# Kernel tuning notes

Measured on AMD Instinct MI355X. Metric: run time of the kernel, lower is better.

Reference implementation:

```python
import jax, jax.numpy as jnp
import numpy as np

HIDDEN = 1024
HEADS = 16
HEAD_DIM = 64
FFN = 4096
LAYERS = 8
QLEN = 9
PATCH = 4
PREFIX = PATCH + 1
LATENT = 64
NSTEPS = 4


def _rope_tables():
    # matches __init__: cos/sin for positions 0..QLEN-1, sin first half negated
    half = HEAD_DIM // 2
    inv = 1.0 / (10000.0 ** (np.arange(half, dtype=np.float64) / half))
    ang = np.arange(QLEN)[:, None] * inv[None, :]          # [QLEN, half]
    cos = np.concatenate([np.cos(ang), np.cos(ang)], -1)   # [QLEN, HEAD_DIM]
    sin = np.concatenate([-np.sin(ang), np.sin(ang)], -1)  # first half *= -1
    return jnp.asarray(cos, jnp.float32), jnp.asarray(sin, jnp.float32)

ROPE_COS, ROPE_SIN = _rope_tables()


def _rms(x):
    # norm weight * sqrt(hidden) is folded into the following projection
    return x * jax.lax.rsqrt(jnp.sum(x * x, -1, keepdims=True))


def setup_inputs() -> dict:
    key = jax.random.key(0)
    ks = jax.random.split(key, 16)
    s = 0.02
    return {
        "step": 2,
        "random": jax.random.normal(ks[0], (1, PATCH, LATENT), jnp.float32),
        "dit_hidden": jax.random.normal(ks[1], (1, 1, HIDDEN), jnp.float32),
        "feat_cond": jax.random.normal(ks[2], (2, PATCH, HIDDEN), jnp.float32),
        "cfg_value": jnp.array([2.5], jnp.float32),
        "cfg_value_minus": jnp.array([1.0 - 2.5], jnp.float32),
        "t_emb": jax.random.normal(ks[3], (NSTEPS, 1, 1, HIDDEN), jnp.float32) * s,
        "dt": jax.random.uniform(ks[4], (NSTEPS,), jnp.float32) * 0.3,
        "in_proj_w": jax.random.normal(ks[5], (HIDDEN, LATENT), jnp.float32) * s,
        "in_proj_b": jnp.zeros((HIDDEN,), jnp.float32),
        "qkv_w": jax.random.normal(ks[6], (LAYERS, 3 * HIDDEN, HIDDEN), jnp.float32) * s,
        "qkv_b": jnp.zeros((LAYERS, 3 * HIDDEN), jnp.float32),
        "o_w": jax.random.normal(ks[7], (LAYERS, HIDDEN, HIDDEN), jnp.float32) * s,
        "gate_up_w": jax.random.normal(ks[8], (LAYERS, 2 * FFN, HIDDEN), jnp.float32) * s,
        "down_w": jax.random.normal(ks[9], (LAYERS, HIDDEN, FFN), jnp.float32) * s,
        "out_proj_w": jax.random.normal(ks[10], (LATENT, HIDDEN), jnp.float32) * s,
        "out_proj_b": jnp.zeros((LATENT,), jnp.float32),
    }


def reference(step, random, dit_hidden, feat_cond, cfg_value, cfg_value_minus,
              t_emb, dt, in_proj_w, in_proj_b, qkv_w, qkv_b, o_w, gate_up_w,
              down_w, out_proj_w, out_proj_b):
    t = t_emb[step]                                     # [1,1,H]
    h = dit_hidden + t
    h = jnp.concatenate([h, t], 0)                      # [2,1,H]  (cond / uncond)
    x = random @ in_proj_w.T + in_proj_b                # [1,PATCH,H]
    x = jnp.concatenate([x, x], 0)                      # [2,PATCH,H]
    hs = jnp.concatenate([h, feat_cond, x], 1)          # [2,QLEN,H]

    for i in range(LAYERS):
        res = hs
        n = _rms(hs)
        qkv = (n @ qkv_w[i].T + qkv_b[i]).reshape(2, QLEN, 3 * HEADS, HEAD_DIM)
        qk, v = qkv[:, :, :2 * HEADS], qkv[:, :, 2 * HEADS:]
        # RoPE (rotate_half = swap halves; sign is in ROPE_SIN)
        x1, x2 = jnp.split(qk, 2, axis=-1)
        rot = jnp.concatenate([x2, x1], -1)
        qk = qk * ROPE_COS[None, :, None, :] + rot * ROPE_SIN[None, :, None, :]
        q, k = qk[:, :, :HEADS], qk[:, :, HEADS:]
        # head_dim**-0.25 scale already folded into q/k weights
        scores = jnp.einsum('bqhd,bkhd->bhqk', q, k)
        attn = jax.nn.softmax(scores, -1)
        o = jnp.einsum('bhqk,bkhd->bqhd', attn, v).reshape(2, QLEN, HIDDEN)
        hs = res + o @ o_w[i].T
        res = hs
        n = _rms(hs)
        gu = n @ gate_up_w[i].T
        g, u = jnp.split(gu, 2, -1)
        hs = res + (jax.nn.silu(g) * u) @ down_w[i].T

    out = _rms(hs[:, PREFIX:]) @ out_proj_w.T + out_proj_b   # [2,PATCH,LATENT]
    pos = out[:1].reshape(1, 1, -1)
    neg = out[1:].reshape(1, 1, -1)
    dot = jnp.sum(pos * neg, -1, keepdims=True)
    sq = jnp.sum(neg * neg, -1, keepdims=True)
    guided = cfg_value * pos + cfg_value_minus * (dot / sq) * neg
    return random + guided.reshape(1, PATCH, LATENT) * dt[step]
```

## Files before the change

kernel.cpp:

```cpp
#include <hip/hip_runtime.h>
#include <hip/hip_bf16.h>

#define ROWS 18
#define HID 1024

__device__ __forceinline__ float dot4(float4 a, float4 b){
  return fmaf(a.x,b.x, fmaf(a.y,b.y, fmaf(a.z,b.z, a.w*b.w)));
}

template<int K, int S, int G, int NC, int ACT, int CSTR, bool RMS, bool BIAS, bool ATOMIC>
__global__ __launch_bounds__(256)
void gemm18(const float* __restrict__ W, const float* __restrict__ act,
            const float* __restrict__ bias, float* __restrict__ out)
{
  constexpr int L   = 64 / G;
  constexpr int KB  = K / S;
  constexpr int PK  = (KB <= 512) ? KB : 512;
  constexpr int NP  = KB / PK;
  constexpr int CHUNK = 4 * L;
  constexpr int NCH = PK / CHUNK;
  constexpr int CPB = 4 * G * NC;

  __shared__ float s_act[ROWS][PK];
  __shared__ float s_red[4 * G * NC * ROWS];
  __shared__ float s_scale[ROWS];

  const int tid  = threadIdx.x;
  const int w    = tid >> 6;
  const int lane = tid & 63;
  const int g    = (G == 1) ? 0 : (lane / L);
  const int l    = (G == 1) ? lane : (lane % L);
  const int cb   = blockIdx.x * CPB + (w * G + g) * NC;
  const int k0   = blockIdx.y * KB;

  float acc[NC][ROWS];
  #pragma unroll
  for (int i = 0; i < NC; i++)
    #pragma unroll
    for (int r = 0; r < ROWS; r++) acc[i][r] = 0.f;

  float rs[5];
  #pragma unroll
  for (int t = 0; t < 5; t++) rs[t] = 0.f;

  for (int p = 0; p < NP; p++) {
    __syncthreads();
    constexpr int N4 = ROWS * PK / 4;
    for (int t4 = tid; t4 < N4; t4 += 256) {
      const int r  = t4 / (PK / 4);
      const int k4 = (t4 % (PK / 4)) * 4;
      const int kg = k0 + p * PK + k4;
      float4 v;
      if (ACT == 0) {
        v = *(const float4*)&act[(size_t)r * K + kg];
      } else {
        float4 gv = *(const float4*)&act[(size_t)r * 8192 + kg];
        float4 uv = *(const float4*)&act[(size_t)r * 8192 + 4096 + kg];
        v.x = gv.x / (1.f + __expf(-gv.x)) * uv.x;
        v.y = gv.y / (1.f + __expf(-gv.y)) * uv.y;
        v.z = gv.z / (1.f + __expf(-gv.z)) * uv.z;
        v.w = gv.w / (1.f + __expf(-gv.w)) * uv.w;
      }
      *(float4*)&s_act[r][k4] = v;
    }
    __syncthreads();

    if (RMS) {
      #pragma unroll
      for (int t = 0; t < 5; t++) {
        const int r = w + 4 * t;
        if (r < ROWS) {
          float ss = 0.f;
          for (int kk = 4 * lane; kk < PK; kk += 256) {
            float4 a = *(const float4*)&s_act[r][kk];
            ss += dot4(a, a);
          }
          rs[t] += ss;
        }
      }
    }

    #pragma unroll
    for (int ch = 0; ch < NCH; ch++) {
      const int kk = ch * CHUNK + 4 * l;
      float4 wv[NC];
      #pragma unroll
      for (int i = 0; i < NC; i++)
        wv[i] = *(const float4*)&W[(size_t)(cb + i) * K + k0 + p * PK + kk];
      #pragma unroll
      for (int r = 0; r < ROWS; r++) {
        float4 a = *(const float4*)&s_act[r][kk];
        #pragma unroll
        for (int i = 0; i < NC; i++)
          acc[i][r] = fmaf(wv[i].x, a.x, fmaf(wv[i].y, a.y,
                      fmaf(wv[i].z, a.z, fmaf(wv[i].w, a.w, acc[i][r]))));
      }
    }
  }

  if (RMS) {
    #pragma unroll
    for (int t = 0; t < 5; t++) {
      const int r = w + 4 * t;
      if (r < ROWS) {
        float ss = rs[t];
        #pragma unroll
        for (int m = 32; m >= 1; m >>= 1) ss += __shfl_xor(ss, m);
        if (lane == 0) s_scale[r] = rsqrtf(ss);
      }
    }
  }

  #pragma unroll
  for (int i = 0; i < NC; i++)
    #pragma unroll
    for (int r = 0; r < ROWS; r++) {
      float v = acc[i][r];
      #pragma unroll
      for (int m = L / 2; m >= 1; m >>= 1) v += __shfl_xor(v, m);
      if (l == 0) s_red[((w * G + g) * NC + i) * ROWS + r] = v;
    }
  __syncthreads();

  constexpr int TOT = 4 * G * NC * ROWS;
  for (int t = tid; t < TOT; t += 256) {
    const int r    = t % ROWS;
    const int rest = t / ROWS;
    const int c    = blockIdx.x * CPB + rest;
    float v = s_red[rest * ROWS + r];
    if (RMS)  v *= s_scale[r];
    if (BIAS) v += bias[c];
    if (ATOMIC) atomicAdd(&out[(size_t)r * CSTR + c], v);
    else        out[(size_t)r * CSTR + c] = v;
  }
}

__global__ __launch_bounds__(256)
void prep_kernel(const int* __restrict__ step, const float* __restrict__ random_,
                 const float* __restrict__ dit_hidden, const float* __restrict__ feat_cond,
                 const float* __restrict__ t_emb, const float* __restrict__ in_w,
                 const float* __restrict__ in_b, float* __restrict__ hs)
{
  const int c = blockIdx.x * 256 + threadIdx.x;
  const int st = step[0];
  const float tv = t_emb[(size_t)st * HID + c];
  hs[0 * HID + c] = dit_hidden[c] + tv;
  hs[9 * HID + c] = tv;
  #pragma unroll
  for (int p = 0; p < 4; p++) {
    hs[(1 + p) * HID + c]     = feat_cond[(0 * 4 + p) * HID + c];
    hs[(9 + 1 + p) * HID + c] = feat_cond[(1 * 4 + p) * HID + c];
  }
  #pragma unroll
  for (int p = 0; p < 4; p++) {
    float a = in_b[c];
    #pragma unroll
    for (int q4 = 0; q4 < 16; q4++) {
      float4 wv = *(const float4*)&in_w[c * 64 + q4 * 4];
      float4 rv = *(const float4*)&random_[p * 64 + q4 * 4];
      a += dot4(wv, rv);
    }
    hs[(5 + p) * HID + c]     = a;
    hs[(9 + 5 + p) * HID + c] = a;
  }
}

__global__ __launch_bounds__(64)
void attn_kernel(const float* __restrict__ qkv, float* __restrict__ attn_out)
{
  const int bh = blockIdx.x;
  const int b = bh >> 4, h = bh & 15;
  const int d = threadIdx.x;
  const float* base = qkv + (size_t)b * 9 * 3072;
  float q[9], k[9], v[9];
  #pragma unroll
  for (int i = 0; i < 9; i++) {
    q[i] = base[i * 3072 + h * 64 + d];
    k[i] = base[i * 3072 + (16 + h) * 64 + d];
    v[i] = base[i * 3072 + (32 + h) * 64 + d];
  }
  const int j = d & 31;
  const float inv = powf(10000.f, -(float)j * (1.f / 32.f));
  #pragma unroll
  for (int i = 0; i < 9; i++) {
    const float ang = (float)i * inv;
    float sn, cs;
    sincosf(ang, &sn, &cs);
    const float sgn = (d < 32) ? -sn : sn;
    const float rq = __shfl_xor(q[i], 32);
    const float rk = __shfl_xor(k[i], 32);
    q[i] = q[i] * cs + rq * sgn;
    k[i] = k[i] * cs + rk * sgn;
  }
  float* obase = attn_out + (size_t)b * 9 * HID + h * 64 + d;
  for (int i = 0; i < 9; i++) {
    float sc[9];
    #pragma unroll
    for (int jj = 0; jj < 9; jj++) {
      float p = q[i] * k[jj];
      #pragma unroll
      for (int m = 32; m >= 1; m >>= 1) p += __shfl_xor(p, m);
      sc[jj] = p;
    }
    float mx = sc[0];
    #pragma unroll
    for (int jj = 1; jj < 9; jj++) mx = fmaxf(mx, sc[jj]);
    float den = 0.f;
    #pragma unroll
    for (int jj = 0; jj < 9; jj++) { sc[jj] = __expf(sc[jj] - mx); den += sc[jj]; }
    float o = 0.f;
    #pragma unroll
    for (int jj = 0; jj < 9; jj++) o += sc[jj] * v[jj];
    obase[i * HID] = o / den;
  }
}

__global__ __launch_bounds__(256)
void outproj_kernel(const float* __restrict__ hs, const float* __restrict__ W,
                    const float* __restrict__ bias, float* __restrict__ out_tmp)
{
  const int c = blockIdx.x, t = threadIdx.x;
  const int w = t >> 6, lane = t & 63;
  const float4 w4 = *(const float4*)&W[(size_t)c * HID + t * 4];
  __shared__ float la[8][4], ls[8][4];
  #pragma unroll
  for (int r8 = 0; r8 < 8; r8++) {
    const int row = (r8 >> 2) * 9 + 5 + (r8 & 3);
    const float4 h4 = *(const float4*)&hs[(size_t)row * HID + t * 4];
    float a = dot4(w4, h4), s = dot4(h4, h4);
    #pragma unroll
    for (int m = 32; m >= 1; m >>= 1) { a += __shfl_xor(a, m); s += __shfl_xor(s, m); }
    if (lane == 0) { la[r8][w] = a; ls[r8][w] = s; }
  }
  __syncthreads();
  if (t < 8) {
    const float a = la[t][0] + la[t][1] + la[t][2] + la[t][3];
    const float s = ls[t][0] + ls[t][1] + ls[t][2] + ls[t][3];
    out_tmp[t * 64 + c] = a * rsqrtf(s) + bias[c];
  }
}

__global__ __launch_bounds__(256)
void combine_kernel(const float* __restrict__ out_tmp, const float* __restrict__ random_,
                    const float* __restrict__ cfg, const float* __restrict__ cfgm,
                    const float* __restrict__ dt, const int* __restrict__ step,
                    float* __restrict__ dout)
{
  const int t = threadIdx.x;
  const int w = t >> 6, lane = t & 63;
  const float pos = out_tmp[t], neg = out_tmp[256 + t];
  float d = pos * neg, s = neg * neg;
  #pragma unroll
  for (int m = 32; m >= 1; m >>= 1) { d += __shfl_xor(d, m); s += __shfl_xor(s, m); }
  __shared__ float ld[4], lsq[4];
  if (lane == 0) { ld[w] = d; lsq[w] = s; }
  __syncthreads();
  const float dot = ld[0] + ld[1] + ld[2] + ld[3];
  const float sq  = lsq[0] + lsq[1] + lsq[2] + lsq[3];
  const float guided = cfg[0] * pos + cfgm[0] * (dot / sq) * neg;
  dout[t] = random_[t] + guided * dt[step[0]];
}

extern "C" void kernel_launch(void* const* d_in, const int* in_sizes, int n_in,
                              void* d_out, int out_size, void* d_ws, size_t ws_size,
                              hipStream_t stream)
{
  const int*   step   = (const int*)  d_in[0];
  const float* random_= (const float*)d_in[1];
  const float* dit_h  = (const float*)d_in[2];
  const float* feat   = (const float*)d_in[3];
  const float* cfg    = (const float*)d_in[4];
  const float* cfgm   = (const float*)d_in[5];
  const float* t_emb  = (const float*)d_in[6];
  const float* dt     = (const float*)d_in[7];
  const float* in_w   = (const float*)d_in[8];
  const float* in_b   = (const float*)d_in[9];
  const float* qkv_w  = (const float*)d_in[10];
  const float* qkv_b  = (const float*)d_in[11];
  const float* o_w    = (const float*)d_in[12];
  const float* gu_w   = (const float*)d_in[13];
  const float* dn_w   = (const float*)d_in[14];
  const float* op_w   = (const float*)d_in[15];
  const float* op_b   = (const float*)d_in[16];

  float* hs     = (float*)d_ws;
  float* qkvb   = hs    + ROWS * HID;
  float* attnb  = qkvb  + ROWS * 3072;
  float* gub    = attnb + ROWS * HID;
  float* outtmp = gub   + ROWS * 8192;

  prep_kernel<<<4, 256, 0, stream>>>(step, random_, dit_h, feat, t_emb, in_w, in_b, hs);

  for (int i = 0; i < 8; i++) {
    const float* qw = qkv_w + (size_t)i * 3072 * 1024;
    const float* qb = qkv_b + (size_t)i * 3072;
    const float* ow = o_w   + (size_t)i * 1024 * 1024;
    const float* gw = gu_w  + (size_t)i * 8192 * 1024;
    const float* dw = dn_w  + (size_t)i * 1024 * 4096;

    gemm18<1024, 1, 1, 4, 0, 3072, true,  true,  false>
        <<<dim3(192, 1), 256, 0, stream>>>(qw, hs, qb, qkvb);
    attn_kernel<<<32, 64, 0, stream>>>(qkvb, attnb);
    gemm18<1024, 4, 1, 4, 0, 1024, false, false, true>
        <<<dim3(64, 4), 256, 0, stream>>>(ow, attnb, nullptr, hs);
    gemm18<1024, 1, 2, 4, 0, 8192, true,  false, false>
        <<<dim3(256, 1), 256, 0, stream>>>(gw, hs, nullptr, gub);
    gemm18<4096, 4, 1, 4, 1, 1024, false, false, true>
        <<<dim3(64, 4), 256, 0, stream>>>(dw, gub, nullptr, hs);
  }

  outproj_kernel<<<64, 256, 0, stream>>>(hs, op_w, op_b, outtmp);
  combine_kernel<<<1, 256, 0, stream>>>(outtmp, random_, cfg, cfgm, dt, step, (float*)d_out);
}
```

Before: 952.5 us.

## Fuse all layers into one persistent cooperative kernel with grid syncs

Replaces the ~42 separate kernel launches (prep, per-layer GEMMs, attention, outproj, combine) with a single cooperative kernel of 256 blocks × 512 threads. Phases are separated by grid.sync() instead of kernel boundaries. The GEMM work split is reworked: one wave per column group with full 64-lane K reduction and different columns-per-wave. This is meant to remove launch overhead and inter-kernel gaps, but grid barriers cost time of their own and the per-block tiling changes how well weight bandwidth is used.

```diff
diff --git a/kernel.cpp b/kernel.cpp
--- a/kernel.cpp
+++ b/kernel.cpp
@@ -1,5 +1,8 @@
 #include <hip/hip_runtime.h>
 #include <hip/hip_bf16.h>
+#include <hip/hip_cooperative_groups.h>
+
+namespace cg = cooperative_groups;
 
 #define ROWS 18
 #define HID 1024
@@ -8,30 +11,17 @@
   return fmaf(a.x,b.x, fmaf(a.y,b.y, fmaf(a.z,b.z, a.w*b.w)));
 }
 
-template<int K, int S, int G, int NC, int ACT, int CSTR, bool RMS, bool BIAS, bool ATOMIC>
-__global__ __launch_bounds__(256)
-void gemm18(const float* __restrict__ W, const float* __restrict__ act,
-            const float* __restrict__ bias, float* __restrict__ out)
+template<int K, int ASTR, int PK, int NP, int NWACT, int NC, int ACT, int CSTR,
+         bool RMS, bool BIAS, bool ATOMIC>
+__device__ __forceinline__ void phase_gemm(
+    const float* __restrict__ Wt, const float* __restrict__ act,
+    const float* __restrict__ bias, float* __restrict__ outp,
+    float* __restrict__ sact, float* __restrict__ sred, float* __restrict__ sscale,
+    int cb, int k0)
 {
-  constexpr int L   = 64 / G;
-  constexpr int KB  = K / S;
-  constexpr int PK  = (KB <= 512) ? KB : 512;
-  constexpr int NP  = KB / PK;
-  constexpr int CHUNK = 4 * L;
-  constexpr int NCH = PK / CHUNK;
-  constexpr int CPB = 4 * G * NC;
-
-  __shared__ float s_act[ROWS][PK];
-  __shared__ float s_red[4 * G * NC * ROWS];
-  __shared__ float s_scale[ROWS];
-
   const int tid  = threadIdx.x;
   const int w    = tid >> 6;
   const int lane = tid & 63;
-  const int g    = (G == 1) ? 0 : (lane / L);
-  const int l    = (G == 1) ? lane : (lane % L);
-  const int cb   = blockIdx.x * CPB + (w * G + g) * NC;
-  const int k0   = blockIdx.y * KB;
 
   float acc[NC][ROWS];
   #pragma unroll
@@ -39,40 +29,39 @@
     #pragma unroll
     for (int r = 0; r < ROWS; r++) acc[i][r] = 0.f;
 
-  float rs[5];
-  #pragma unroll
-  for (int t = 0; t < 5; t++) rs[t] = 0.f;
+  float rs[3] = {0.f, 0.f, 0.f};
 
   for (int p = 0; p < NP; p++) {
     __syncthreads();
     constexpr int N4 = ROWS * PK / 4;
-    for (int t4 = tid; t4 < N4; t4 += 256) {
+    for (int t4 = tid; t4 < N4; t4 += 512) {
       const int r  = t4 / (PK / 4);
       const int k4 = (t4 % (PK / 4)) * 4;
       const int kg = k0 + p * PK + k4;
       float4 v;
       if (ACT == 0) {
-        v = *(const float4*)&act[(size_t)r * K + kg];
+        v = *(const float4*)&act[(size_t)r * ASTR + kg];
       } else {
-        float4 gv = *(const float4*)&act[(size_t)r * 8192 + kg];
-        float4 uv = *(const float4*)&act[(size_t)r * 8192 + 4096 + kg];
+        float4 gv = *(const float4*)&act[(size_t)r * ASTR + kg];
+        float4 uv = *(const float4*)&act[(size_t)r * ASTR + 4096 + kg];
         v.x = gv.x / (1.f + __expf(-gv.x)) * uv.x;
         v.y = gv.y / (1.f + __expf(-gv.y)) * uv.y;
         v.z = gv.z / (1.f + __expf(-gv.z)) * uv.z;
         v.w = gv.w / (1.f + __expf(-gv.w)) * uv.w;
       }
-      *(float4*)&s_act[r][k4] = v;
+      *(float4*)&sact[r * PK + k4] = v;
     }
     __syncthreads();
 
     if (RMS) {
       #pragma unroll
-      for (int t = 0; t < 5; t++) {
-        const int r = w + 4 * t;
+      for (int t = 0; t < 3; t++) {
+        const int r = w + 8 * t;
         if (r < ROWS) {
           float ss = 0.f;
+          #pragma unroll
           for (int kk = 4 * lane; kk < PK; kk += 256) {
-            float4 a = *(const float4*)&s_act[r][kk];
+            float4 a = *(const float4*)&sact[r * PK + kk];
             ss += dot4(a, a);
           }
           rs[t] += ss;
@@ -80,216 +69,114 @@
       }
     }
 
-    #pragma unroll
-    for (int ch = 0; ch < NCH; ch++) {
-      const int kk = ch * CHUNK + 4 * l;
-      float4 wv[NC];
-      #pragma unroll
-      for (int i = 0; i < NC; i++)
-        wv[i] = *(const float4*)&W[(size_t)(cb + i) * K + k0 + p * PK + kk];
-      #pragma unroll
-      for (int r = 0; r < ROWS; r++) {
-        float4 a = *(const float4*)&s_act[r][kk];
+    if (w < NWACT) {
+      constexpr int NCH = PK / 256;
+      #pragma unroll
+      for (int ch = 0; ch < NCH; ch++) {
+        const int kk = ch * 256 + 4 * lane;
+        float4 wv[NC];
         #pragma unroll
         for (int i = 0; i < NC; i++)
-          acc[i][r] = fmaf(wv[i].x, a.x, fmaf(wv[i].y, a.y,
-                      fmaf(wv[i].z, a.z, fmaf(wv[i].w, a.w, acc[i][r]))));
+          wv[i] = *(const float4*)&Wt[(size_t)(cb + w * NC + i) * K + k0 + p * PK + kk];
+        #pragma unroll
+        for (int r = 0; r < ROWS; r++) {
+          float4 a = *(const float4*)&sact[r * PK + kk];
+          #pragma unroll
+          for (int i = 0; i < NC; i++)
+            acc[i][r] = fmaf(wv[i].x, a.x, fmaf(wv[i].y, a.y,
+                        fmaf(wv[i].z, a.z, fmaf(wv[i].w, a.w, acc[i][r]))));
+        }
       }
     }
   }
 
   if (RMS) {
     #pragma unroll
-    for (int t = 0; t < 5; t++) {
-      const int r = w + 4 * t;
+    for (int t = 0; t < 3; t++) {
+      const int r = w + 8 * t;
       if (r < ROWS) {
         float ss = rs[t];
         #pragma unroll
         for (int m = 32; m >= 1; m >>= 1) ss += __shfl_xor(ss, m);
-        if (lane == 0) s_scale[r] = rsqrtf(ss);
-      }
-    }
-  }
-
-  #pragma unroll
-  for (int i = 0; i < NC; i++)
-    #pragma unroll
-    for (int r = 0; r < ROWS; r++) {
-      float v = acc[i][r];
-      #pragma unroll
-      for (int m = L / 2; m >= 1; m >>= 1) v += __shfl_xor(v, m);
-      if (l == 0) s_red[((w * G + g) * NC + i) * ROWS + r] = v;
-    }
+        if (lane == 0) sscale[r] = rsqrtf(ss);
+      }
+    }
+  }
+
+  if (w < NWACT) {
+    #pragma unroll
+    for (int i = 0; i < NC; i++)
+      #pragma unroll
+      for (int r = 0; r < ROWS; r++) {
+        float v = acc[i][r];
+        #pragma unroll
+        for (int m = 32; m >= 1; m >>= 1) v += __shfl_xor(v, m);
+        if (lane == 0) sred[(w * NC + i) * ROWS + r] = v;
+      }
+  }
   __syncthreads();
 
-  constexpr int TOT = 4 * G * NC * ROWS;
-  for (int t = tid; t < TOT; t += 256) {
+  constexpr int TOT = NWACT * NC * ROWS;
+  for (int t = tid; t < TOT; t += 512) {
     const int r    = t % ROWS;
     const int rest = t / ROWS;
-    const int c    = blockIdx.x * CPB + rest;
-    float v = s_red[rest * ROWS + r];
-    if (RMS)  v *= s_scale[r];
+    const int c    = cb + rest;
+    float v = sred[rest * ROWS + r];
+    if (RMS)  v *= sscale[r];
     if (BIAS) v += bias[c];
-    if (ATOMIC) atomicAdd(&out[(size_t)r * CSTR + c], v);
-    else        out[(size_t)r * CSTR + c] = v;
+    if (ATOMIC) atomicAdd(&outp[(size_t)r * CSTR + c], v);
+    else        outp[(size_t)r * CSTR + c] = v;
   }
 }
 
-__global__ __launch_bounds__(256)
-void prep_kernel(const int* __restrict__ step, const float* __restrict__ random_,
-                 const float* __restrict__ dit_hidden, const float* __restrict__ feat_cond,
-                 const float* __restrict__ t_emb, const float* __restrict__ in_w,
-                 const float* __restrict__ in_b, float* __restrict__ hs)
+__global__ __launch_bounds__(512, 2)
+void voxcpm_fused(const int* __restrict__ step, const float* __restrict__ random_,
+                  const float* __restrict__ dit_h, const float* __restrict__ feat,
+                  const float* __restrict__ cfg, const float* __restrict__ cfgm,
+                  const float* __restrict__ t_emb, const float* __restrict__ dt,
+                  const float* __restrict__ in_w, const float* __restrict__ in_b,
+                  const float* __restrict__ qkv_w, const float* __restrict__ qkv_b,
+                  const float* __restrict__ o_w, const float* __restrict__ gu_w,
+                  const float* __restrict__ dn_w, const float* __restrict__ op_w,
+                  const float* __restrict__ op_b,
+                  float* __restrict__ hs, float* __restrict__ qkvb,
+                  float* __restrict__ attnb, float* __restrict__ gub,
+                  float* __restrict__ outtmp, float* __restrict__ dout)
 {
-  const int c = blockIdx.x * 256 + threadIdx.x;
-  const int st = step[0];
-  const float tv = t_emb[(size_t)st * HID + c];
-  hs[0 * HID + c] = dit_hidden[c] + tv;
-  hs[9 * HID + c] = tv;
-  #pragma unroll
-  for (int p = 0; p < 4; p++) {
-    hs[(1 + p) * HID + c]     = feat_cond[(0 * 4 + p) * HID + c];
-    hs[(9 + 1 + p) * HID + c] = feat_cond[(1 * 4 + p) * HID + c];
-  }
-  #pragma unroll
-  for (int p = 0; p < 4; p++) {
-    float a = in_b[c];
-    #pragma unroll
-    for (int q4 = 0; q4 < 16; q4++) {
-      float4 wv = *(const float4*)&in_w[c * 64 + q4 * 4];
-      float4 rv = *(const float4*)&random_[p * 64 + q4 * 4];
-      a += dot4(wv, rv);
-    }
-    hs[(5 + p) * HID + c]     = a;
-    hs[(9 + 5 + p) * HID + c] = a;
-  }
-}
-
-__global__ __launch_bounds__(64)
-void attn_kernel(const float* __restrict__ qkv, float* __restrict__ attn_out)
-{
-  const int bh = blockIdx.x;
-  const int b = bh >> 4, h = bh & 15;
-  const int d = threadIdx.x;
-  const float* base = qkv + (size_t)b * 9 * 3072;
-  float q[9], k[9], v[9];
-  #pragma unroll
-  for (int i = 0; i < 9; i++) {
-    q[i] = base[i * 3072 + h * 64 + d];
-    k[i] = base[i * 3072 + (16 + h) * 64 + d];
-    v[i] = base[i * 3072 + (32 + h) * 64 + d];
-  }
-  const int j = d & 31;
-  const float inv = powf(10000.f, -(float)j * (1.f / 32.f));
-  #pragma unroll
-  for (int i = 0; i < 9; i++) {
-    const float ang = (float)i * inv;
-    float sn, cs;
-    sincosf(ang, &sn, &cs);
-    const float sgn = (d < 32) ? -sn : sn;
-    const float rq = __shfl_xor(q[i], 32);
-    const float rk = __shfl_xor(k[i], 32);
-    q[i] = q[i] * cs + rq * sgn;
-    k[i] = k[i] * cs + rk * sgn;
-  }
-  float* obase = attn_out + (size_t)b * 9 * HID + h * 64 + d;
-  for (int i = 0; i < 9; i++) {
-    float sc[9];
-    #pragma unroll
-    for (int jj = 0; jj < 9; jj++) {
-      float p = q[i] * k[jj];
-      #pragma unroll
-      for (int m = 32; m >= 1; m >>= 1) p += __shfl_xor(p, m);
-      sc[jj] = p;
-    }
-    float mx = sc[0];
-    #pragma unroll
-    for (int jj = 1; jj < 9; jj++) mx = fmaxf(mx, sc[jj]);
-    float den = 0.f;
-    #pragma unroll
-    for (int jj = 0; jj < 9; jj++) { sc[jj] = __expf(sc[jj] - mx); den += sc[jj]; }
-    float o = 0.f;
-    #pragma unroll
-    for (int jj = 0; jj < 9; jj++) o += sc[jj] * v[jj];
-    obase[i * HID] = o / den;
-  }
-}
-
-__global__ __launch_bounds__(256)
-void outproj_kernel(const float* __restrict__ hs, const float* __restrict__ W,
-                    const float* __restrict__ bias, float* __restrict__ out_tmp)
-{
-  const int c = blockIdx.x, t = threadIdx.x;
-  const int w = t >> 6, lane = t & 63;
-  const float4 w4 = *(const float4*)&W[(size_t)c * HID + t * 4];
-  __shared__ float la[8][4], ls[8][4];
-  #pragma unroll
-  for (int r8 = 0; r8 < 8; r8++) {
-    const int row = (r8 >> 2) * 9 + 5 + (r8 & 3);
-    const float4 h4 = *(const float4*)&hs[(size_t)row * HID + t * 4];
-    float a = dot4(w4, h4), s = dot4(h4, h4);
-    #pragma unroll
-    for (int m = 32; m >= 1; m >>= 1) { a += __shfl_xor(a, m); s += __shfl_xor(s, m); }
-    if (lane == 0) { la[r8][w] = a; ls[r8][w] = s; }
-  }
-  __syncthreads();
-  if (t < 8) {
-    const float a = la[t][0] + la[t][1] + la[t][2] + la[t][3];
-    const float s = ls[t][0] + ls[t][1] + ls[t][2] + ls[t][3];
-    out_tmp[t * 64 + c] = a * rsqrtf(s) + bias[c];
-  }
-}
-
-__global__ __launch_bounds__(256)
-void combine_kernel(const float* __restrict__ out_tmp, const float* __restrict__ random_,
-                    const float* __restrict__ cfg, const float* __restrict__ cfgm,
-                    const float* __restrict__ dt, const int* __restrict__ step,
-                    float* __restrict__ dout)
-{
-  const int t = threadIdx.x;
-  const int w = t >> 6, lane = t & 63;
-  const float pos = out_tmp[t], neg = out_tmp[256 + t];
-  float d = pos * neg, s = neg * neg;
-  #pragma unroll
-  for (int m = 32; m >= 1; m >>= 1) { d += __shfl_xor(d, m); s += __shfl_xor(s, m); }
-  __shared__ float ld[4], lsq[4];
-  if (lane == 0) { ld[w] = d; lsq[w] = s; }
-  __syncthreads();
-  const float dot = ld[0] + ld[1] + ld[2] + ld[3];
-  const float sq  = lsq[0] + lsq[1] + lsq[2] + lsq[3];
-  const float guided = cfg[0] * pos + cfgm[0] * (dot / sq) * neg;
-  dout[t] = random_[t] + guided * dt[step[0]];
-}
-
-extern "C" void kernel_launch(void* const* d_in, const int* in_sizes, int n_in,
-                              void* d_out, int out_size, void* d_ws, size_t ws_size,
-                              hipStream_t stream)
-{
-  const int*   step   = (const int*)  d_in[0];
-  const float* random_= (const float*)d_in[1];
-  const float* dit_h  = (const float*)d_in[2];
-  const float* feat   = (const float*)d_in[3];
-  const float* cfg    = (const float*)d_in[4];
-  const float* cfgm   = (const float*)d_in[5];
-  const float* t_emb  = (const float*)d_in[6];
-  const float* dt     = (const float*)d_in[7];
-  const float* in_w   = (const float*)d_in[8];
-  const float* in_b   = (const float*)d_in[9];
-  const float* qkv_w  = (const float*)d_in[10];
-  const float* qkv_b  = (const float*)d_in[11];
-  const float* o_w    = (const float*)d_in[12];
-  const float* gu_w   = (const float*)d_in[13];
-  const float* dn_w   = (const float*)d_in[14];
-  const float* op_w   = (const float*)d_in[15];
-  const float* op_b   = (const float*)d_in[16];
-
-  float* hs     = (float*)d_ws;
-  float* qkvb   = hs    + ROWS * HID;
-  float* attnb  = qkvb  + ROWS * 3072;
-  float* gub    = attnb + ROWS * HID;
-  float* outtmp = gub   + ROWS * 8192;
-
-  prep_kernel<<<4, 256, 0, stream>>>(step, random_, dit_h, feat, t_emb, in_w, in_b, hs);
+  cg::grid_group grid = cg::this_grid();
+  __shared__ float sact[ROWS * 512];
+  __shared__ float sred[8 * 4 * ROWS];
+  __shared__ float sscale[ROWS];
+  __shared__ float smisc[144];
+
+  const int b   = blockIdx.x;
+  const int tid = threadIdx.x;
+
+  if (b < 2) {
+    const int c  = b * 512 + tid;
+    const int st = step[0];
+    const float tv = t_emb[(size_t)st * HID + c];
+    hs[0 * HID + c] = dit_h[c] + tv;
+    hs[9 * HID + c] = tv;
+    #pragma unroll
+    for (int p = 0; p < 4; p++) {
+      hs[(1 + p) * HID + c]  = feat[(size_t)(0 * 4 + p) * HID + c];
+      hs[(10 + p) * HID + c] = feat[(size_t)(1 * 4 + p) * HID + c];
+    }
+    #pragma unroll
+    for (int p = 0; p < 4; p++) {
+      float a = in_b[c];
+      #pragma unroll
+      for (int q4 = 0; q4 < 16; q4++) {
+        float4 wv = *(const float4*)&in_w[(size_t)c * 64 + q4 * 4];
+        float4 rv = *(const float4*)&random_[p * 64 + q4 * 4];
+        a += dot4(wv, rv);
+      }
+      hs[(5 + p) * HID + c]  = a;
+      hs[(14 + p) * HID + c] = a;
+    }
+  }
+  grid.sync();
 
   for (int i = 0; i < 8; i++) {
     const float* qw = qkv_w + (size_t)i * 3072 * 1024;
@@ -298,17 +185,156 @@
     const float* gw = gu_w  + (size_t)i * 8192 * 1024;
     const float* dw = dn_w  + (size_t)i * 1024 * 4096;
 
-    gemm18<1024, 1, 1, 4, 0, 3072, true,  true,  false>
-        <<<dim3(192, 1), 256, 0, stream>>>(qw, hs, qb, qkvb);
-    attn_kernel<<<32, 64, 0, stream>>>(qkvb, attnb);
-    gemm18<1024, 4, 1, 4, 0, 1024, false, false, true>
-        <<<dim3(64, 4), 256, 0, stream>>>(ow, attnb, nullptr, hs);
-    gemm18<1024, 1, 2, 4, 0, 8192, true,  false, false>
-        <<<dim3(256, 1), 256, 0, stream>>>(gw, hs, nullptr, gub);
-    gemm18<4096, 4, 1, 4, 1, 1024, false, false, true>
-        <<<dim3(64, 4), 256, 0, stream>>>(dw, gub, nullptr, hs);
-  }
-
-  outproj_kernel<<<64, 256, 0, stream>>>(hs, op_w, op_b, outtmp);
-  combine_kernel<<<1, 256, 0, stream>>>(outtmp, random_, cfg, cfgm, dt, step, (float*)d_out);
+    phase_gemm<1024, 1024, 512, 2, 6, 2, 0, 3072, true, true, false>
+        (qw, hs, qb, qkvb, sact, sred, sscale, b * 12, 0);
+    grid.sync();
+
+    if (b < 32 && tid < 64) {
+      const int bb = b >> 4, h = b & 15, d = tid;
+      const float* base = qkvb + (size_t)bb * 9 * 3072;
+      float q[9], k[9], v[9];
+      #pragma unroll
+      for (int ii = 0; ii < 9; ii++) {
+        q[ii] = base[ii * 3072 + h * 64 + d];
+        k[ii] = base[ii * 3072 + (16 + h) * 64 + d];
+        v[ii] = base[ii * 3072 + (32 + h) * 64 + d];
+      }
+      const int j = d & 31;
+      const float inv = powf(10000.f, -(float)j * (1.f / 32.f));
+      #pragma unroll
+      for (int ii = 0; ii < 9; ii++) {
+        const float ang = (float)ii * inv;
+        float sn, cs;
+        __sincosf(ang, &sn, &cs);
+        const float sgn = (d < 32) ? -sn : sn;
+        const float rq = __shfl_xor(q[ii], 32);
+        const float rk = __shfl_xor(k[ii], 32);
+        q[ii] = q[ii] * cs + rq * sgn;
+        k[ii] = k[ii] * cs + rk * sgn;
+      }
+      float* obase = attnb + (size_t)bb * 9 * HID + h * 64 + d;
+      for (int ii = 0; ii < 9; ii++) {
+        float sc[9];
+        #pragma unroll
+        for (int jj = 0; jj < 9; jj++) {
+          float p = q[ii] * k[jj];
+          #pragma unroll
+          for (int m = 32; m >= 1; m >>= 1) p += __shfl_xor(p, m);
+          sc[jj] = p;
+        }
+        float mx = sc[0];
+        #pragma unroll
+        for (int jj = 1; jj < 9; jj++) mx = fmaxf(mx, sc[jj]);
+        float den = 0.f;
+        #pragma unroll
+        for (int jj = 0; jj < 9; jj++) { sc[jj] = __expf(sc[jj] - mx); den += sc[jj]; }
+        float o = 0.f;
+        #pragma unroll
+        for (int jj = 0; jj < 9; jj++) o += sc[jj] * v[jj];
+        obase[ii * HID] = o / den;
+      }
+    }
+    grid.sync();
+
+    phase_gemm<1024, 1024, 256, 1, 8, 2, 0, 1024, false, false, true>
+        (ow, attnb, nullptr, hs, sact, sred, sscale, (b & 63) * 16, (b >> 6) * 256);
+    grid.sync();
+
+    phase_gemm<1024, 1024, 512, 2, 8, 4, 0, 8192, true, false, false>
+        (gw, hs, nullptr, gub, sact, sred, sscale, b * 32, 0);
+    grid.sync();
+
+    phase_gemm<4096, 8192, 512, 2, 8, 2, 1, 1024, false, false, true>
+        (dw, gub, nullptr, hs, sact, sred, sscale, (b & 63) * 16, (b >> 6) * 1024);
+    grid.sync();
+  }
+
+  if (b < 64) {
+    const int c = b;
+    const int w = tid >> 6, lane = tid & 63;
+    float* la = smisc;
+    float* ls = smisc + 64;
+    const float2 wv = ((const float2*)&op_w[(size_t)c * HID])[tid];
+    #pragma unroll
+    for (int r8 = 0; r8 < 8; r8++) {
+      const int row = (r8 >> 2) * 9 + 5 + (r8 & 3);
+      const float2 hv = ((const float2*)&hs[(size_t)row * HID])[tid];
+      float a = fmaf(wv.x, hv.x, wv.y * hv.y);
+      float s = fmaf(hv.x, hv.x, hv.y * hv.y);
+      #pragma unroll
+      for (int m = 32; m >= 1; m >>= 1) { a += __shfl_xor(a, m); s += __shfl_xor(s, m); }
+      if (lane == 0) { la[r8 * 8 + w] = a; ls[r8 * 8 + w] = s; }
+    }
+    __syncthreads();
+    if (tid < 8) {
+      float a = 0.f, s = 0.f;
+      #pragma unroll
+      for (int jj = 0; jj < 8; jj++) { a += la[tid * 8 + jj]; s += ls[tid * 8 + jj]; }
+      outtmp[tid * 64 + c] = a * rsqrtf(s) + op_b[c];
+    }
+  }
+  grid.sync();
+
+  if (b == 0) {
+    const int w = tid >> 6, lane = tid & 63;
+    float pos = 0.f, neg = 0.f, d = 0.f, s = 0.f;
+    if (tid < 256) {
+      pos = outtmp[tid]; neg = outtmp[256 + tid];
+      d = pos * neg; s = neg * neg;
+    }
+    #pragma unroll
+    for (int m = 32; m >= 1; m >>= 1) { d += __shfl_xor(d, m); s += __shfl_xor(s, m); }
+    float* ld  = smisc;
+    float* lsq = smisc + 8;
+    if (lane == 0) { ld[w] = d; lsq[w] = s; }
+    __syncthreads();
+    if (tid < 256) {
+      float dot = 0.f, sq = 0.f;
+      #pragma unroll
+      for (int jj = 0; jj < 8; jj++) { dot += ld[jj]; sq += lsq[jj]; }
+      const float guided = cfg[0] * pos + cfgm[0] * (dot / sq) * neg;
+      dout[tid] = random_[tid] + guided * dt[step[0]];
+    }
+  }
 }
+
+extern "C" void kernel_launch(void* const* d_in, const int* in_sizes, int n_in,
+                              void* d_out, int out_size, void* d_ws, size_t ws_size,
+                              hipStream_t stream)
+{
+  const int*   step    = (const int*)  d_in[0];
+  const float* random_ = (const float*)d_in[1];
+  const float* dit_h   = (const float*)d_in[2];
+  const float* feat    = (const float*)d_in[3];
+  const float* cfg     = (const float*)d_in[4];
+  const float* cfgm    = (const float*)d_in[5];
+  const float* t_emb   = (const float*)d_in[6];
+  const float* dt      = (const float*)d_in[7];
+  const float* in_w    = (const float*)d_in[8];
+  const float* in_b    = (const float*)d_in[9];
+  const float* qkv_w   = (const float*)d_in[10];
+  const float* qkv_b   = (const float*)d_in[11];
+  const float* o_w     = (const float*)d_in[12];
+  const float* gu_w    = (const float*)d_in[13];
+  const float* dn_w    = (const float*)d_in[14];
+  const float* op_w    = (const float*)d_in[15];
+  const float* op_b    = (const float*)d_in[16];
+
+  float* hs     = (float*)d_ws;
+  float* qkvb   = hs    + ROWS * HID;
+  float* attnb  = qkvb  + ROWS * 3072;
+  float* gub    = attnb + ROWS * HID;
+  float* outtmp = gub   + ROWS * 8192;
+  float* dout   = (float*)d_out;
+
+  void* args[] = {
+    (void*)&step, (void*)&random_, (void*)&dit_h, (void*)&feat, (void*)&cfg,
+    (void*)&cfgm, (void*)&t_emb, (void*)&dt, (void*)&in_w, (void*)&in_b,
+    (void*)&qkv_w, (void*)&qkv_b, (void*)&o_w, (void*)&gu_w, (void*)&dn_w,
+    (void*)&op_w, (void*)&op_b,
+    (void*)&hs, (void*)&qkvb, (void*)&attnb, (void*)&gub, (void*)&outtmp,
+    (void*)&dout
+  };
+  hipLaunchCooperativeKernel((void*)voxcpm_fused, dim3(256), dim3(512),
+                             args, 0, stream);
+}
```

New measurement: 1.838 ms. 93.0% more time.
